# Kernel optimization log

Measured on AMD Instinct MI355X. Metric: run time of the kernel, lower is better.

## Reference

```python
import jax, jax.numpy as jnp
import numpy as np

NEG_SLOPE = 0.2
NUM_NODES = 100000
NUM_EDGES = 200000
NNZ = 1600000
IN_C = 128
OUT_C = 128
STAR = 64


def setup_inputs() -> dict:
    key = jax.random.key(0)
    ks = jax.random.split(key, 12)
    X = jax.random.normal(ks[0], (NUM_NODES, IN_C), dtype=jnp.float32)
    V = jax.random.randint(ks[1], (NNZ,), 0, NUM_NODES)
    E = jax.random.randint(ks[2], (NNZ,), 0, NUM_EDGES)
    S_features = jax.random.normal(ks[3], (NUM_EDGES, STAR), dtype=jnp.float32)
    s = 1.0 / np.sqrt(IN_C)
    Wx = jax.random.uniform(ks[4], (IN_C, OUT_C), minval=-s, maxval=s)
    bx = jax.random.uniform(ks[5], (OUT_C,), minval=-s, maxval=s)
    Wv = jax.random.uniform(ks[6], (IN_C, OUT_C), minval=-s, maxval=s)
    bv = jax.random.uniform(ks[7], (OUT_C,), minval=-s, maxval=s)
    sa = 1.0 / np.sqrt(OUT_C)
    a_vec = jax.random.uniform(ks[8], (OUT_C,), minval=-sa, maxval=sa)
    st = 1.0 / np.sqrt(OUT_C + STAR)
    Wt = jax.random.uniform(ks[9], (OUT_C + STAR, OUT_C), minval=-st, maxval=st)
    bt = jax.random.uniform(ks[10], (OUT_C,), minval=-st, maxval=st)
    return {"X": X, "V": V, "E": E, "S_features": S_features,
            "Wx": Wx, "bx": bx, "Wv": Wv, "bv": bv,
            "a_vec": a_vec, "Wt": Wt, "bt": bt}


def _segment_softmax(s, seg, num_segments):
    m = jax.ops.segment_max(s, seg, num_segments=num_segments)
    e = jnp.exp(s - m[seg])
    denom = jax.ops.segment_sum(e, seg, num_segments=num_segments)
    return e / denom[seg]


def reference(X, V, E, S_features, Wx, bx, Wv, bv, a_vec, Wt, bt):
    # DPHGNNConv forward (eval mode: dropout = identity)
    X_init = X @ Wx + bx                      # [N, out]
    X_feat = X @ Wv + bv                      # [N, out]
    scores = X_feat @ a_vec                   # [N]
    s = jax.nn.leaky_relu(scores[V], NEG_SLOPE)  # [nnz]
    w = _segment_softmax(s, E, NUM_EDGES)     # [nnz]
    Xev = X_feat[V] * w[:, None]              # [nnz, out]
    Y_v2e = jax.ops.segment_sum(Xev, E, num_segments=NUM_EDGES)
    Y_v2e = jax.nn.elu(Y_v2e)
    e_msg = jnp.concatenate([Y_v2e, S_features], axis=1)  # [E, out+star]
    Y = e_msg @ Wt + bt                       # [E, out]
    Yev = Y[E]                                # [nnz, out]
    num = jax.ops.segment_sum(Yev, V, num_segments=NUM_NODES)
    cnt = jax.ops.segment_sum(jnp.ones((NNZ,), jnp.float32), V, num_segments=NUM_NODES)
    Xn = num / jnp.maximum(cnt, 1.0)[:, None]  # scatter_mean
    Xn = jax.nn.elu(Xn)                        # is_last=False
    return Xn + X_init
```

## Files before the change

### kernel.cpp

```cpp
#include <hip/hip_runtime.h>
#include <math.h>

#define N_NODES 100000
#define N_EDGES 200000
#define NNZ_    1600000
#define INC  128
#define OUTC 128
#define STAR_ 64
#define NEG 0.2f
#define NBIN_E 391
#define NBIN_V 196
#define NBIN (NBIN_E + NBIN_V)
#define CHUNK 4000
#define NBLK_A (NNZ_/CHUNK)
#define CAP_E 5120
#define CAP_V 9216
#define PAIR_SZ (NBIN_E*CAP_E + NBIN_V*CAP_V)
#define CAPI 288
#define CAPN 288

typedef __attribute__((ext_vector_type(8))) short bf16x8_t;
typedef __attribute__((ext_vector_type(8))) unsigned short u16x8;
typedef __attribute__((ext_vector_type(4))) float f32x4_t;

__device__ __forceinline__ float leaky(float x){ return x > 0.f ? x : NEG*x; }
__device__ __forceinline__ float elu1(float x){ return x > 0.f ? x : __expf(x)-1.f; }
__device__ __forceinline__ unsigned short f2bf(float f){
  unsigned u = __float_as_uint(f);
  unsigned r = u + 0x7FFFu + ((u >> 16) & 1u);
  return (unsigned short)(r >> 16);
}
__device__ __forceinline__ float bf2f(unsigned short h){
  return __uint_as_float(((unsigned)h) << 16);
}
__device__ __forceinline__ int padBaseD(int bin){
  return bin < NBIN_E ? bin*CAP_E : NBIN_E*CAP_E + (bin-NBIN_E)*CAP_V;
}

__global__ void k_cvt(const float* __restrict__ Wx, const float* __restrict__ Wv,
                      const float* __restrict__ Wt,
                      unsigned short* __restrict__ WcatT, unsigned short* __restrict__ WtT,
                      int* __restrict__ binCur,
                      int* __restrict__ vIdxE, int* __restrict__ eIdxV){
  const int i = blockIdx.x*256 + threadIdx.x;
  if (i < 256*128){
    const int n = i >> 7, k = i & 127;
    const float v = (n < 128) ? Wx[k*128 + n] : Wv[k*128 + (n-128)];
    WcatT[n*128 + k] = f2bf(v);
  }
  const int j = i - 256*128;
  if (j >= 0 && j < 128*192){
    const int n = j / 192, k = j - n*192;
    WtT[n*192 + k] = f2bf(Wt[k*128 + n]);
  }
  if (blockIdx.x == 0){
    for (int p = threadIdx.x; p < NBIN; p += 256) binCur[p] = padBaseD(p);
    if (threadIdx.x < 16){ vIdxE[NNZ_ + threadIdx.x] = 0; eIdxV[NNZ_ + threadIdx.x] = 0; }
  }
}

__global__ __launch_bounds__(256) void k_front(
    const float* __restrict__ X, const unsigned short* __restrict__ WcatT,
    const float* __restrict__ bx, const float* __restrict__ bv,
    const float* __restrict__ av,
    float* __restrict__ Xinit, unsigned short* __restrict__ Xfb,
    float* __restrict__ scoresExp,
    const int* __restrict__ V, const int* __restrict__ E,
    int* __restrict__ binCur, int2* __restrict__ pair){
  __shared__ int hA[NBIN];
  __shared__ int baseA[NBIN];
  __shared__ unsigned short xb[16][136];
  __shared__ float sc[16];
  const int tid = threadIdx.x;

  if (blockIdx.x < NBLK_A) {
    for (int p = tid; p < NBIN; p += 256) hA[p] = 0;
    __syncthreads();
    const int start = blockIdx.x*CHUNK, end = start + CHUNK;
    for (int i = start + tid; i < end; i += 256){
      atomicAdd(&hA[E[i] >> 9], 1);
      atomicAdd(&hA[NBIN_E + (V[i] >> 9)], 1);
    }
    __syncthreads();
    for (int p = tid; p < NBIN; p += 256)
      baseA[p] = hA[p] ? atomicAdd(&binCur[p], hA[p]) : 0;
    __syncthreads();
    for (int p = tid; p < NBIN; p += 256) hA[p] = 0;
    __syncthreads();
    for (int i = start + tid; i < end; i += 256){
      const int e = E[i], v = V[i];
      const int be = e >> 9, bv_ = NBIN_E + (v >> 9);
      const int se = baseA[be]  + atomicAdd(&hA[be],  1);
      const int sv = baseA[bv_] + atomicAdd(&hA[bv_], 1);
      pair[se] = make_int2(e, v);
      pair[sv] = make_int2(v, e);
    }
    return;
  }

  const int lane = tid & 63, w = tid >> 6;
  const int quad = lane >> 4, l16 = lane & 15;
  const int r0 = (blockIdx.x - NBLK_A) * 16;
  if (tid < 16) sc[tid] = 0.f;
  {
    const int r = tid >> 4;
    const int c0 = (tid & 15) * 8;
    const float4 a4 = *(const float4*)&X[(size_t)(r0+r)*INC + c0];
    const float4 b4 = *(const float4*)&X[(size_t)(r0+r)*INC + c0 + 4];
    bf16x8_t pk;
    pk[0]=(short)f2bf(a4.x); pk[1]=(short)f2bf(a4.y); pk[2]=(short)f2bf(a4.z); pk[3]=(short)f2bf(a4.w);
    pk[4]=(short)f2bf(b4.x); pk[5]=(short)f2bf(b4.y); pk[6]=(short)f2bf(b4.z); pk[7]=(short)f2bf(b4.w);
    *(bf16x8_t*)&xb[r][c0] = pk;
  }
  __syncthreads();
  f32x4_t acc[4] = {{0,0,0,0},{0,0,0,0},{0,0,0,0},{0,0,0,0}};
  const int n_base = w*64 + l16;
  for (int s = 0; s < 4; ++s){
    const bf16x8_t af = *(const bf16x8_t*)&xb[l16][s*32 + quad*8];
    #pragma unroll
    for (int nt = 0; nt < 4; ++nt){
      const int n = n_base + nt*16;
      const bf16x8_t bf = *(const bf16x8_t*)&WcatT[(size_t)n*128 + s*32 + quad*8];
      acc[nt] = __builtin_amdgcn_mfma_f32_16x16x32_bf16(af, bf, acc[nt], 0, 0, 0);
    }
  }
  float pr[4] = {0.f, 0.f, 0.f, 0.f};
  #pragma unroll
  for (int nt = 0; nt < 4; ++nt){
    const int n = n_base + nt*16;
    const float bias = (n < 128) ? bx[n] : bv[n-128];
    #pragma unroll
    for (int r = 0; r < 4; ++r){
      const int m = quad*4 + r;
      const float val = acc[nt][r] + bias;
      if (n < 128) Xinit[(size_t)(r0+m)*OUTC + n] = val;
      else {
        Xfb[(size_t)(r0+m)*OUTC + (n-128)] = f2bf(val);
        pr[r] += val * av[n-128];
      }
    }
  }
  if (w >= 2){
    #pragma unroll
    for (int r = 0; r < 4; ++r) atomicAdd(&sc[quad*4 + r], pr[r]);
  }
  __syncthreads();
  if (tid < 16) scoresExp[r0 + tid] = __expf(leaky(sc[tid]));
}

__global__ __launch_bounds__(512) void k_binBE(const int2* __restrict__ pair,
    const int* __restrict__ binCur,
    int* __restrict__ vIdxE, int* __restrict__ cntE, int* __restrict__ startsE){
  __shared__ int h[512], sc0[512], sc1[512];
  const int bin = blockIdx.x;
  const int bucket0 = bin << 9;
  const int pstart = padBaseD(bin);
  const int n = binCur[bin] - pstart;
  const int tid = threadIdx.x;
  {
    int part = 0;
    for (int p = tid; p < bin; p += 512) part += binCur[p] - padBaseD(p);
    sc0[tid] = part;
    __syncthreads();
    for (int o = 256; o; o >>= 1){ if (tid < o) sc0[tid] += sc0[tid+o]; __syncthreads(); }
  }
  const int itemBase = sc0[0];
  __syncthreads();
  h[tid] = 0;
  __syncthreads();
  for (int j = tid; j < n; j += 512) atomicAdd(&h[pair[pstart + j].x & 511], 1);
  __syncthreads();
  sc0[tid] = h[tid];
  __syncthreads();
  int* a = sc0; int* b = sc1;
  for (int o = 1; o < 512; o <<= 1){
    b[tid] = a[tid] + (tid >= o ? a[tid-o] : 0);
    __syncthreads();
    int* t = a; a = b; b = t;
  }
  {
    const int excl = a[tid] - h[tid];
    b[tid] = itemBase + excl;
    const int bucket = bucket0 + tid;
    if (bucket < N_EDGES){ cntE[bucket] = h[tid]; startsE[bucket] = itemBase + excl; }
  }
  __syncthreads();
  for (int j = tid; j < n; j += 512){
    const int2 kv = pair[pstart + j];
    const int slot = atomicAdd(&b[kv.x & 511], 1);
    vIdxE[slot] = kv.y;
  }
}

__global__ __launch_bounds__(256) void k_edgeV(
    const int* __restrict__ cntE, const int* __restrict__ startsE,
    const int* __restrict__ vIdxE, const float* __restrict__ scoresExp,
    const unsigned short* __restrict__ Xfb,
    const float* __restrict__ S, const unsigned short* __restrict__ WtT,
    const float* __restrict__ bt, unsigned short* __restrict__ Ybf,
    const int2* __restrict__ pair, const int* __restrict__ binCur,
    int* __restrict__ eIdxV, int* __restrict__ cntV, int* __restrict__ startsV) {
  __shared__ __align__(16) char smem[(CAPI + 8)*4 + 16*200*2];
  const int tid = threadIdx.x;

  if (blockIdx.x < NBIN_V) {
    int* h   = (int*)smem;
    int* sc0 = h + 512;
    int* sc1 = sc0 + 512;
    const int nb = blockIdx.x;
    const int bin = NBIN_E + nb;
    const int bucket0 = nb << 9;
    const int pstart = padBaseD(bin);
    const int n = binCur[bin] - pstart;
    {
      int part = 0;
      for (int p = tid; p < bin; p += 256) part += binCur[p] - padBaseD(p);
      sc0[tid] = part;
      __syncthreads();
      for (int o = 128; o; o >>= 1){ if (tid < o) sc0[tid] += sc0[tid+o]; __syncthreads(); }
    }
    const int itemBase = sc0[0] - NNZ_;
    __syncthreads();
    for (int p = tid; p < 512; p += 256) h[p] = 0;
    __syncthreads();
    for (int j = tid; j < n; j += 256) atomicAdd(&h[pair[pstart + j].x & 511], 1);
    __syncthreads();
    for (int p = tid; p < 512; p += 256) sc0[p] = h[p];
    __syncthreads();
    int* a = sc0; int* b = sc1;
    for (int o = 1; o < 512; o <<= 1){
      for (int p = tid; p < 512; p += 256) b[p] = a[p] + (p >= o ? a[p-o] : 0);
      __syncthreads();
      int* t = a; a = b; b = t;
    }
    for (int p = tid; p < 512; p += 256){
      const int excl = a[p] - h[p];
      b[p] = itemBase + excl;
      const int bucket = bucket0 + p;
      if (bucket < N_NODES){ cntV[bucket] = h[p]; startsV[bucket] = itemBase + excl; }
    }
    __syncthreads();
    for (int j = tid; j < n; j += 256){
      const int2 kv = pair[pstart + j];
      const int slot = atomicAdd(&b[kv.x & 511], 1);
      eIdxV[slot] = kv.y;
    }
    return;
  }

  int* inc = (int*)smem;
  unsigned short (*msg)[200] = (unsigned short (*)[200])(smem + (CAPI + 8)*4);
  const int lane = tid & 63, w = tid >> 6;
  const int e0 = (blockIdx.x - NBIN_V) * 16;
  const int g16 = tid >> 4, s16 = tid & 15;

  const int st0 = startsE[e0];
  const int lim = startsE[e0 + 15] + cntE[e0 + 15] - st0;

  for (int i = tid; i < CAPI + 8; i += 256)
    inc[i] = (i < lim) ? vIdxE[st0 + i] : 0;

  {
    const float4 s4 = *(const float4*)&S[(size_t)(e0+g16)*STAR_ + s16*4];
    ushort4 pk; pk.x=f2bf(s4.x); pk.y=f2bf(s4.y); pk.z=f2bf(s4.z); pk.w=f2bf(s4.w);
    *(ushort4*)&msg[g16][128 + s16*4] = pk;
  }
  __syncthreads();

  const int e = e0 + g16;
  const int deg = cntE[e];
  const int lo  = startsE[e] - st0;
  const int c8 = s16 * 8;
  float ac[8] = {0.f,0.f,0.f,0.f,0.f,0.f,0.f,0.f};
  float wsum = 0.f;
  if (lo + deg <= CAPI) {
    for (int j = 0; j < deg; j += 8) {
      int pp[8];
      #pragma unroll
      for (int k = 0; k < 8; ++k) pp[k] = inc[lo + j + k];
      float ww[8];
      #pragma unroll
      for (int k = 0; k < 8; ++k) ww[k] = scoresExp[pp[k]];
      u16x8 xx[8];
      #pragma unroll
      for (int k = 0; k < 8; ++k)
        xx[k] = *(const u16x8*)&Xfb[(size_t)pp[k]*OUTC + c8];
      #pragma unroll
      for (int k = 0; k < 8; ++k) {
        const float wgt = (j + k < deg) ? ww[k] : 0.f;
        wsum += wgt;
        #pragma unroll
        for (int q = 0; q < 8; ++q) ac[q] += wgt * bf2f(xx[k][q]);
      }
    }
  } else {
    const int st = st0 + lo;
    for (int j = 0; j < deg; j += 8) {
      int pp[8];
      #pragma unroll
      for (int k = 0; k < 8; ++k) pp[k] = vIdxE[st + j + k];
      float ww[8];
      #pragma unroll
      for (int k = 0; k < 8; ++k) ww[k] = scoresExp[pp[k]];
      u16x8 xx[8];
      #pragma unroll
      for (int k = 0; k < 8; ++k)
        xx[k] = *(const u16x8*)&Xfb[(size_t)pp[k]*OUTC + c8];
      #pragma unroll
      for (int k = 0; k < 8; ++k) {
        const float wgt = (j + k < deg) ? ww[k] : 0.f;
        wsum += wgt;
        #pragma unroll
        for (int q = 0; q < 8; ++q) ac[q] += wgt * bf2f(xx[k][q]);
      }
    }
  }
  {
    const float invd = wsum > 0.f ? 1.f/wsum : 0.f;
    u16x8 pk;
    #pragma unroll
    for (int q = 0; q < 8; ++q) pk[q] = f2bf(elu1(ac[q]*invd));
    *(u16x8*)&msg[g16][c8] = pk;
  }
  __syncthreads();

  const int quad = lane >> 4, l16 = lane & 15;
  f32x4_t acc0 = {0,0,0,0}, acc1 = {0,0,0,0};
  const int n0 = w * 32;
  for (int s = 0; s < 6; ++s) {
    const bf16x8_t af = *(const bf16x8_t*)&msg[l16][s*32 + quad*8];
    const bf16x8_t b0 = *(const bf16x8_t*)&WtT[(size_t)(n0 + l16)*192      + s*32 + quad*8];
    const bf16x8_t b1 = *(const bf16x8_t*)&WtT[(size_t)(n0 + 16 + l16)*192 + s*32 + quad*8];
    acc0 = __builtin_amdgcn_mfma_f32_16x16x32_bf16(af, b0, acc0, 0, 0, 0);
    acc1 = __builtin_amdgcn_mfma_f32_16x16x32_bf16(af, b1, acc1, 0, 0, 0);
  }
  const float bt0 = bt[n0 + l16], bt1 = bt[n0 + 16 + l16];
  #pragma unroll
  for (int r = 0; r < 4; ++r) {
    const int m = quad*4 + r;
    Ybf[(size_t)(e0+m)*OUTC + n0 + l16]      = f2bf(acc0[r] + bt0);
    Ybf[(size_t)(e0+m)*OUTC + n0 + 16 + l16] = f2bf(acc1[r] + bt1);
  }
}

__global__ __launch_bounds__(256) void k_node(
    const int* __restrict__ cntV, const int* __restrict__ startsV,
    const int* __restrict__ eIdxV,
    const unsigned short* __restrict__ Ybf, float* __restrict__ out) {
  __shared__ int elds[CAPN + 8];
  const int tid = threadIdx.x;
  const int sub = tid & 31, grp = tid >> 5;
  const int v0 = blockIdx.x * 8;

  const int st0 = startsV[v0];
  const int lim = startsV[v0 + 7] + cntV[v0 + 7] - st0;
  for (int i = tid; i < CAPN + 8; i += 256)
    elds[i] = (i < lim) ? eIdxV[st0 + i] : 0;
  __syncthreads();

  const int v = v0 + grp;
  const int c4 = sub * 4;
  const int deg = cntV[v];
  const int lo  = startsV[v] - st0;
  float a0=0.f, a1=0.f, a2=0.f, a3=0.f;
  if (lo + deg <= CAPN) {
    for (int j = 0; j < deg; j += 8) {
      int ee[8];
      #pragma unroll
      for (int k = 0; k < 8; ++k) ee[k] = elds[lo + j + k];
      ushort4 yy[8];
      #pragma unroll
      for (int k = 0; k < 8; ++k)
        yy[k] = *(const ushort4*)&Ybf[(size_t)ee[k]*OUTC + c4];
      #pragma unroll
      for (int k = 0; k < 8; ++k) {
        const float pz = (j + k < deg) ? 1.f : 0.f;
        a0 += pz * bf2f(yy[k].x); a1 += pz * bf2f(yy[k].y);
        a2 += pz * bf2f(yy[k].z); a3 += pz * bf2f(yy[k].w);
      }
    }
  } else {
    const int st = st0 + lo;
    for (int j = 0; j < deg; j += 8) {
      int ee[8];
      #pragma unroll
      for (int k = 0; k < 8; ++k) ee[k] = eIdxV[st + j + k];
      ushort4 yy[8];
      #pragma unroll
      for (int k = 0; k < 8; ++k)
        yy[k] = *(const ushort4*)&Ybf[(size_t)ee[k]*OUTC + c4];
      #pragma unroll
      for (int k = 0; k < 8; ++k) {
        const float pz = (j + k < deg) ? 1.f : 0.f;
        a0 += pz * bf2f(yy[k].x); a1 += pz * bf2f(yy[k].y);
        a2 += pz * bf2f(yy[k].z); a3 += pz * bf2f(yy[k].w);
      }
    }
  }
  const float invd = 1.f / fmaxf((float)deg, 1.f);
  float4 o = *(float4*)&out[(size_t)v*OUTC + c4];
  o.x = elu1(a0*invd) + o.x;
  o.y = elu1(a1*invd) + o.y;
  o.z = elu1(a2*invd) + o.z;
  o.w = elu1(a3*invd) + o.w;
  *(float4*)&out[(size_t)v*OUTC + c4] = o;
}

extern "C" void kernel_launch(void* const* d_in, const int* in_sizes, int n_in,
                              void* d_out, int out_size, void* d_ws, size_t ws_size,
                              hipStream_t stream) {
  const float* X  = (const float*)d_in[0];
  const int*   V  = (const int*)d_in[1];
  const int*   E  = (const int*)d_in[2];
  const float* S  = (const float*)d_in[3];
  const float* Wx = (const float*)d_in[4];
  const float* bx = (const float*)d_in[5];
  const float* Wv = (const float*)d_in[6];
  const float* bv = (const float*)d_in[7];
  const float* av = (const float*)d_in[8];
  const float* Wt = (const float*)d_in[9];
  const float* bt = (const float*)d_in[10];
  float* out = (float*)d_out;

  char* ws = (char*)d_ws;
  size_t off = 0;
  auto alloc = [&](size_t bytes) -> void* {
    off = (off + 255) & ~(size_t)255;
    void* p = ws + off; off += bytes; return p;
  };
  unsigned short* Xfb   = (unsigned short*)alloc((size_t)N_NODES*OUTC*2);
  unsigned short* Ybf   = (unsigned short*)alloc((size_t)N_EDGES*OUTC*2);
  float* scoresExp = (float*)alloc((size_t)N_NODES*4);
  unsigned short* WcatT = (unsigned short*)alloc((size_t)256*128*2);
  unsigned short* WtT   = (unsigned short*)alloc((size_t)128*192*2);
  int2* pair   = (int2*)alloc((size_t)PAIR_SZ*8);
  int* binCur  = (int*)alloc((size_t)NBIN*4);
  int* cntE    = (int*)alloc((size_t)N_EDGES*4);
  int* cntV    = (int*)alloc((size_t)N_NODES*4);
  int* startsE = (int*)alloc((size_t)N_EDGES*4);
  int* startsV = (int*)alloc((size_t)N_NODES*4);
  int* vIdxE   = (int*)alloc((size_t)(NNZ_+16)*4);
  int* eIdxV   = (int*)alloc((size_t)(NNZ_+16)*4);

  k_cvt<<<(256*128 + 128*192 + 255)/256, 256, 0, stream>>>(Wx, Wv, Wt, WcatT, WtT,
                                                           binCur, vIdxE, eIdxV);
  k_front<<<NBLK_A + N_NODES/16, 256, 0, stream>>>(X, WcatT, bx, bv, av, out, Xfb, scoresExp,
                                                   V, E, binCur, pair);
  k_binBE<<<NBIN_E, 512, 0, stream>>>(pair, binCur, vIdxE, cntE, startsE);
  k_edgeV<<<NBIN_V + N_EDGES/16, 256, 0, stream>>>(cntE, startsE, vIdxE, scoresExp,
                                                   Xfb, S, WtT, bt, Ybf,
                                                   pair, binCur, eIdxV, cntV, startsV);
  k_node<<<N_NODES/8, 256, 0, stream>>>(cntV, startsV, eIdxV, Ybf, out);
}
```

Before: 464.6 us.

## Restructure kernel schedule: fuse binning passes with front GEMM, weight conversion with scatter

```diff
diff --git a/kernel.cpp b/kernel.cpp
--- a/kernel.cpp
+++ b/kernel.cpp
@@ -13,6 +13,7 @@
 #define NBIN (NBIN_E + NBIN_V)
 #define CHUNK 4000
 #define NBLK_A (NNZ_/CHUNK)
+#define NBLK_CVT 224
 #define CAP_E 5120
 #define CAP_V 9216
 #define PAIR_SZ (NBIN_E*CAP_E + NBIN_V*CAP_V)
@@ -37,40 +38,15 @@
   return bin < NBIN_E ? bin*CAP_E : NBIN_E*CAP_E + (bin-NBIN_E)*CAP_V;
 }
 
-__global__ void k_cvt(const float* __restrict__ Wx, const float* __restrict__ Wv,
-                      const float* __restrict__ Wt,
-                      unsigned short* __restrict__ WcatT, unsigned short* __restrict__ WtT,
-                      int* __restrict__ binCur,
-                      int* __restrict__ vIdxE, int* __restrict__ eIdxV){
-  const int i = blockIdx.x*256 + threadIdx.x;
-  if (i < 256*128){
-    const int n = i >> 7, k = i & 127;
-    const float v = (n < 128) ? Wx[k*128 + n] : Wv[k*128 + (n-128)];
-    WcatT[n*128 + k] = f2bf(v);
-  }
-  const int j = i - 256*128;
-  if (j >= 0 && j < 128*192){
-    const int n = j / 192, k = j - n*192;
-    WtT[n*192 + k] = f2bf(Wt[k*128 + n]);
-  }
-  if (blockIdx.x == 0){
-    for (int p = threadIdx.x; p < NBIN; p += 256) binCur[p] = padBaseD(p);
-    if (threadIdx.x < 16){ vIdxE[NNZ_ + threadIdx.x] = 0; eIdxV[NNZ_ + threadIdx.x] = 0; }
-  }
-}
-
-__global__ __launch_bounds__(256) void k_front(
-    const float* __restrict__ X, const unsigned short* __restrict__ WcatT,
-    const float* __restrict__ bx, const float* __restrict__ bv,
-    const float* __restrict__ av,
-    float* __restrict__ Xinit, unsigned short* __restrict__ Xfb,
-    float* __restrict__ scoresExp,
+__global__ __launch_bounds__(256) void k_cvtA(
+    const float* __restrict__ Wx, const float* __restrict__ Wv,
+    const float* __restrict__ Wt,
+    unsigned short* __restrict__ WcatT, unsigned short* __restrict__ WtT,
     const int* __restrict__ V, const int* __restrict__ E,
-    int* __restrict__ binCur, int2* __restrict__ pair){
+    int* __restrict__ binCur, int2* __restrict__ pair,
+    int* __restrict__ vIdxE, int* __restrict__ eIdxV){
   __shared__ int hA[NBIN];
   __shared__ int baseA[NBIN];
-  __shared__ unsigned short xb[16][136];
-  __shared__ float sc[16];
   const int tid = threadIdx.x;
 
   if (blockIdx.x < NBLK_A) {
@@ -83,7 +59,7 @@
     }
     __syncthreads();
     for (int p = tid; p < NBIN; p += 256)
-      baseA[p] = hA[p] ? atomicAdd(&binCur[p], hA[p]) : 0;
+      baseA[p] = hA[p] ? padBaseD(p) + atomicAdd(&binCur[p], hA[p]) : 0;
     __syncthreads();
     for (int p = tid; p < NBIN; p += 256) hA[p] = 0;
     __syncthreads();
@@ -98,9 +74,89 @@
     return;
   }
 
+  const int i = (blockIdx.x - NBLK_A)*256 + tid;
+  if (i < 256*128){
+    const int n = i >> 7, k = i & 127;
+    const float v = (n < 128) ? Wx[k*128 + n] : Wv[k*128 + (n-128)];
+    WcatT[n*128 + k] = f2bf(v);
+  }
+  const int j = i - 256*128;
+  if (j >= 0 && j < 128*192){
+    const int n = j / 192, k = j - n*192;
+    WtT[n*192 + k] = f2bf(Wt[k*128 + n]);
+  }
+  if (blockIdx.x == NBLK_A && tid < 16){
+    vIdxE[NNZ_ + tid] = 0; eIdxV[NNZ_ + tid] = 0;
+  }
+}
+
+__global__ __launch_bounds__(256) void k_front2(
+    const float* __restrict__ X, const unsigned short* __restrict__ WcatT,
+    const float* __restrict__ bx, const float* __restrict__ bv,
+    const float* __restrict__ av,
+    float* __restrict__ Xinit, unsigned short* __restrict__ Xfb,
+    float* __restrict__ scoresExp,
+    const int2* __restrict__ pair, const int* __restrict__ binCur,
+    int* __restrict__ vIdxE, int* __restrict__ cntE, int* __restrict__ startsE,
+    int* __restrict__ eIdxV, int* __restrict__ cntV, int* __restrict__ startsV){
+  __shared__ __align__(16) char smem[6144];
+  const int tid = threadIdx.x;
+
+  if (blockIdx.x < NBIN) {
+    int* h   = (int*)smem;
+    int* sc0 = h + 512;
+    int* sc1 = sc0 + 512;
+    const int bin = blockIdx.x;
+    const bool isE = bin < NBIN_E;
+    const int nb = isE ? bin : bin - NBIN_E;
+    const int bucket0 = nb << 9;
+    const int nBuckTot = isE ? N_EDGES : N_NODES;
+    const int pstart = padBaseD(bin);
+    const int n = binCur[bin];
+    {
+      int part = 0;
+      for (int p = tid; p < bin; p += 256) part += binCur[p];
+      sc0[tid] = part;
+      __syncthreads();
+      for (int o = 128; o; o >>= 1){ if (tid < o) sc0[tid] += sc0[tid+o]; __syncthreads(); }
+    }
+    const int itemBase = isE ? sc0[0] : sc0[0] - NNZ_;
+    __syncthreads();
+    for (int p = tid; p < 512; p += 256) h[p] = 0;
+    __syncthreads();
+    for (int j = tid; j < n; j += 256) atomicAdd(&h[pair[pstart + j].x & 511], 1);
+    __syncthreads();
+    for (int p = tid; p < 512; p += 256) sc0[p] = h[p];
+    __syncthreads();
+    int* a = sc0; int* b = sc1;
+    for (int o = 1; o < 512; o <<= 1){
+      for (int p = tid; p < 512; p += 256) b[p] = a[p] + (p >= o ? a[p-o] : 0);
+      __syncthreads();
+      int* t = a; a = b; b = t;
+    }
+    for (int p = tid; p < 512; p += 256){
+      const int excl = a[p] - h[p];
+      b[p] = itemBase + excl;
+      const int bucket = bucket0 + p;
+      if (bucket < nBuckTot){
+        if (isE){ cntE[bucket] = h[p]; startsE[bucket] = itemBase + excl; }
+        else    { cntV[bucket] = h[p]; startsV[bucket] = itemBase + excl; }
+      }
+    }
+    __syncthreads();
+    for (int j = tid; j < n; j += 256){
+      const int2 kv = pair[pstart + j];
+      const int slot = atomicAdd(&b[kv.x & 511], 1);
+      if (isE) vIdxE[slot] = kv.y; else eIdxV[slot] = kv.y;
+    }
+    return;
+  }
+
+  unsigned short (*xb)[136] = (unsigned short (*)[136])smem;
+  float* sc = (float*)(smem + 4352);
   const int lane = tid & 63, w = tid >> 6;
   const int quad = lane >> 4, l16 = lane & 15;
-  const int r0 = (blockIdx.x - NBLK_A) * 16;
+  const int r0 = (blockIdx.x - NBIN) * 16;
   if (tid < 16) sc[tid] = 0.f;
   {
     const int r = tid >> 4;
@@ -148,110 +204,17 @@
   if (tid < 16) scoresExp[r0 + tid] = __expf(leaky(sc[tid]));
 }
 
-__global__ __launch_bounds__(512) void k_binBE(const int2* __restrict__ pair,
-    const int* __restrict__ binCur,
-    int* __restrict__ vIdxE, int* __restrict__ cntE, int* __restrict__ startsE){
-  __shared__ int h[512], sc0[512], sc1[512];
-  const int bin = blockIdx.x;
-  const int bucket0 = bin << 9;
-  const int pstart = padBaseD(bin);
-  const int n = binCur[bin] - pstart;
-  const int tid = threadIdx.x;
-  {
-    int part = 0;
-    for (int p = tid; p < bin; p += 512) part += binCur[p] - padBaseD(p);
-    sc0[tid] = part;
-    __syncthreads();
-    for (int o = 256; o; o >>= 1){ if (tid < o) sc0[tid] += sc0[tid+o]; __syncthreads(); }
-  }
-  const int itemBase = sc0[0];
-  __syncthreads();
-  h[tid] = 0;
-  __syncthreads();
-  for (int j = tid; j < n; j += 512) atomicAdd(&h[pair[pstart + j].x & 511], 1);
-  __syncthreads();
-  sc0[tid] = h[tid];
-  __syncthreads();
-  int* a = sc0; int* b = sc1;
-  for (int o = 1; o < 512; o <<= 1){
-    b[tid] = a[tid] + (tid >= o ? a[tid-o] : 0);
-    __syncthreads();
-    int* t = a; a = b; b = t;
-  }
-  {
-    const int excl = a[tid] - h[tid];
-    b[tid] = itemBase + excl;
-    const int bucket = bucket0 + tid;
-    if (bucket < N_EDGES){ cntE[bucket] = h[tid]; startsE[bucket] = itemBase + excl; }
-  }
-  __syncthreads();
-  for (int j = tid; j < n; j += 512){
-    const int2 kv = pair[pstart + j];
-    const int slot = atomicAdd(&b[kv.x & 511], 1);
-    vIdxE[slot] = kv.y;
-  }
-}
-
-__global__ __launch_bounds__(256) void k_edgeV(
+__global__ __launch_bounds__(256) void k_edge(
     const int* __restrict__ cntE, const int* __restrict__ startsE,
     const int* __restrict__ vIdxE, const float* __restrict__ scoresExp,
     const unsigned short* __restrict__ Xfb,
     const float* __restrict__ S, const unsigned short* __restrict__ WtT,
-    const float* __restrict__ bt, unsigned short* __restrict__ Ybf,
-    const int2* __restrict__ pair, const int* __restrict__ binCur,
-    int* __restrict__ eIdxV, int* __restrict__ cntV, int* __restrict__ startsV) {
-  __shared__ __align__(16) char smem[(CAPI + 8)*4 + 16*200*2];
+    const float* __restrict__ bt, unsigned short* __restrict__ Ybf) {
+  __shared__ int inc[CAPI + 8];
+  __shared__ unsigned short msg[16][200];
   const int tid = threadIdx.x;
-
-  if (blockIdx.x < NBIN_V) {
-    int* h   = (int*)smem;
-    int* sc0 = h + 512;
-    int* sc1 = sc0 + 512;
-    const int nb = blockIdx.x;
-    const int bin = NBIN_E + nb;
-    const int bucket0 = nb << 9;
-    const int pstart = padBaseD(bin);
-    const int n = binCur[bin] - pstart;
-    {
-      int part = 0;
-      for (int p = tid; p < bin; p += 256) part += binCur[p] - padBaseD(p);
-      sc0[tid] = part;
-      __syncthreads();
-      for (int o = 128; o; o >>= 1){ if (tid < o) sc0[tid] += sc0[tid+o]; __syncthreads(); }
-    }
-    const int itemBase = sc0[0] - NNZ_;
-    __syncthreads();
-    for (int p = tid; p < 512; p += 256) h[p] = 0;
-    __syncthreads();
-    for (int j = tid; j < n; j += 256) atomicAdd(&h[pair[pstart + j].x & 511], 1);
-    __syncthreads();
-    for (int p = tid; p < 512; p += 256) sc0[p] = h[p];
-    __syncthreads();
-    int* a = sc0; int* b = sc1;
-    for (int o = 1; o < 512; o <<= 1){
-      for (int p = tid; p < 512; p += 256) b[p] = a[p] + (p >= o ? a[p-o] : 0);
-      __syncthreads();
-      int* t = a; a = b; b = t;
-    }
-    for (int p = tid; p < 512; p += 256){
-      const int excl = a[p] - h[p];
-      b[p] = itemBase + excl;
-      const int bucket = bucket0 + p;
-      if (bucket < N_NODES){ cntV[bucket] = h[p]; startsV[bucket] = itemBase + excl; }
-    }
-    __syncthreads();
-    for (int j = tid; j < n; j += 256){
-      const int2 kv = pair[pstart + j];
-      const int slot = atomicAdd(&b[kv.x & 511], 1);
-      eIdxV[slot] = kv.y;
-    }
-    return;
-  }
-
-  int* inc = (int*)smem;
-  unsigned short (*msg)[200] = (unsigned short (*)[200])(smem + (CAPI + 8)*4);
   const int lane = tid & 63, w = tid >> 6;
-  const int e0 = (blockIdx.x - NBIN_V) * 16;
+  const int e0 = blockIdx.x * 16;
   const int g16 = tid >> 4, s16 = tid & 15;
 
   const int st0 = startsE[e0];
@@ -442,13 +405,14 @@
   int* vIdxE   = (int*)alloc((size_t)(NNZ_+16)*4);
   int* eIdxV   = (int*)alloc((size_t)(NNZ_+16)*4);
 
-  k_cvt<<<(256*128 + 128*192 + 255)/256, 256, 0, stream>>>(Wx, Wv, Wt, WcatT, WtT,
-                                                           binCur, vIdxE, eIdxV);
-  k_front<<<NBLK_A + N_NODES/16, 256, 0, stream>>>(X, WcatT, bx, bv, av, out, Xfb, scoresExp,
-                                                   V, E, binCur, pair);
-  k_binBE<<<NBIN_E, 512, 0, stream>>>(pair, binCur, vIdxE, cntE, startsE);
-  k_edgeV<<<NBIN_V + N_EDGES/16, 256, 0, stream>>>(cntE, startsE, vIdxE, scoresExp,
-                                                   Xfb, S, WtT, bt, Ybf,
-                                                   pair, binCur, eIdxV, cntV, startsV);
+  hipMemsetAsync(binCur, 0, (size_t)NBIN*4, stream);
+  k_cvtA<<<NBLK_A + NBLK_CVT, 256, 0, stream>>>(Wx, Wv, Wt, WcatT, WtT,
+                                                V, E, binCur, pair, vIdxE, eIdxV);
+  k_front2<<<NBIN + N_NODES/16, 256, 0, stream>>>(X, WcatT, bx, bv, av, out, Xfb, scoresExp,
+                                                  pair, binCur,
+                                                  vIdxE, cntE, startsE,
+                                                  eIdxV, cntV, startsV);
+  k_edge<<<N_EDGES/16, 256, 0, stream>>>(cntE, startsE, vIdxE, scoresExp,
+                                         Xfb, S, WtT, bt, Ybf);
   k_node<<<N_NODES/8, 256, 0, stream>>>(cntV, startsV, eIdxV, Ybf, out);
 }
```

Measured after the change: 473.3 us. No clear change (+1.9%).
